# Performance work log

Hardware: AMD Instinct MI355X
Metric: run time of the kernel (lower is better)

## Reference

```python
import jax, jax.numpy as jnp
import numpy as np
import math

B, DIM, H, W = 16, 384, 64, 64
SCALES, HEADS, HID = 4, 4, 32
WIDTH = DIM // SCALES
NUMS = SCALES - 1
PH = PW = 2
LS = 1e-6


def setup_inputs():
    ks = jax.random.split(jax.random.key(0), 20)
    n = lambda i, shape, s=0.02: jax.random.normal(ks[i], shape, jnp.float32) * s
    return {
        'x': jax.random.normal(ks[0], (B, DIM, H, W), jnp.float32),
        'convs_w': n(1, (NUMS, WIDTH, 3, 3)), 'convs_b': n(2, (NUMS, WIDTH)),
        'pos_w': n(3, (DIM, 2 * HID)), 'pos_b': n(4, (DIM,)),
        'ln_xca_w': jnp.ones((DIM,), jnp.float32), 'ln_xca_b': jnp.zeros((DIM,), jnp.float32),
        'gamma_xca': jnp.full((DIM,), LS, jnp.float32),
        'xca_temp': jnp.ones((HEADS, 1, 1), jnp.float32),
        'xca_kv_w': n(5, (2 * DIM, DIM)), 'xca_kv_b': n(6, (2 * DIM,)),
        'xca_proj_w': n(7, (DIM, DIM)), 'xca_proj_b': n(8, (DIM,)),
        'conv_out_w': n(9, (DIM,)), 'conv_out_b': n(10, (DIM,)),
        'wa_kv_w': n(11, (2 * DIM, DIM)), 'wa_kv_b': n(12, (2 * DIM,)),
        'wa_proj_w': n(13, (DIM, DIM)), 'wa_proj_b': n(14, (DIM,)),
        'ln_w': jnp.ones((DIM,), jnp.float32), 'ln_b': jnp.zeros((DIM,), jnp.float32),
        'pw1_w': n(15, (4 * DIM, DIM)), 'pw1_b': n(16, (4 * DIM,)),
        'pw2_w': n(17, (DIM, 4 * DIM)), 'pw2_b': n(18, (DIM,)),
        'gamma': jnp.full((DIM,), LS, jnp.float32),
    }


def layer_norm(x, w, b, eps=1e-6):
    m = jnp.mean(x, -1, keepdims=True)
    v = jnp.mean((x - m) ** 2, -1, keepdims=True)
    return (x - m) * jax.lax.rsqrt(v + eps) * w + b


def l2norm(x, eps=1e-12):  # torch F.normalize over last dim
    return x / jnp.maximum(jnp.linalg.norm(x, axis=-1, keepdims=True), eps)


def dwconv3x3(x, w, b):  # depthwise: w [Cw,3,3]
    out = jax.lax.conv_general_dilated(x, w[:, None], (1, 1), ((1, 1), (1, 1)),
        dimension_numbers=('NCHW', 'OIHW', 'NCHW'), feature_group_count=w.shape[0])
    return out + b[None, :, None, None]


def pos_fourier(pos_w, pos_b):  # -> [H*W, DIM] (batch-independent since mask is all-false)
    scale = 2 * math.pi
    y = jnp.arange(1, H + 1, dtype=jnp.float32)[:, None] / (H + 1e-6) * scale
    xg = jnp.arange(1, W + 1, dtype=jnp.float32)[None, :] / (W + 1e-6) * scale
    y = jnp.broadcast_to(y, (H, W))
    xg = jnp.broadcast_to(xg, (H, W))
    dim_t = jnp.arange(HID, dtype=jnp.float32)
    dim_t = 10000.0 ** (2 * jnp.floor(dim_t / 2) / HID)
    px = xg[..., None] / dim_t
    py = y[..., None] / dim_t
    px = jnp.stack((jnp.sin(px[..., 0::2]), jnp.cos(px[..., 1::2])), -1).reshape(H, W, HID)
    py = jnp.stack((jnp.sin(py[..., 0::2]), jnp.cos(py[..., 1::2])), -1).reshape(H, W, HID)
    pos = jnp.concatenate((py, px), -1)  # [H,W,2*HID]
    return (pos @ pos_w.T + pos_b).reshape(H * W, DIM)


def xca_fn(x, const, kv_w, kv_b, proj_w, proj_b, temp):
    b, n, c = x.shape
    h, hd = HEADS, c // HEADS
    q1 = const.reshape(b, n, h, hd).transpose(0, 2, 3, 1)          # b,h,hd,n
    kv = (x @ kv_w.T + kv_b).reshape(b, n, 2, h, hd).transpose(2, 0, 3, 1, 4)
    k = l2norm(kv[0].transpose(0, 1, 3, 2))                        # b,h,hd,n (L2 over n)
    v = kv[1].transpose(0, 1, 3, 2)                                # b,h,hd,n
    attn = jax.nn.softmax(jnp.einsum('bhcn,bhdn->bhcd', q1, k) * temp, -1)
    out = jnp.einsum('bhcd,bhdn->bhcn', attn, v)
    out = out.transpose(0, 3, 1, 2).reshape(b, n, c)
    return out @ proj_w.T + proj_b


def window_attn(x, const, kv_w, kv_b, proj_w, proj_b):
    b, n, c = x.shape
    h, hd = HEADS, c // HEADS
    kv = (x @ kv_w.T + kv_b).reshape(b, n, 2, h, hd).transpose(2, 0, 3, 1, 4)
    k = l2norm(kv[0].transpose(0, 1, 3, 2))                        # b,h,hd,n
    v = kv[1].transpose(0, 1, 3, 2)                                # b,h,hd,n
    q1 = const.reshape(b, n, 1, h, hd).transpose(2, 0, 3, 1, 4)    # 1,b,h,n,hd (leading 1 kept, as in torch)
    q1 = q1.transpose(0, 1, 2, 4, 3)                               # 1,b,h,hd,n
    logits = jnp.einsum('obhcn,bhdn->obhcd', q1, k)
    attn = 0.5 * logits / math.sqrt(hd) + 0.5 * jax.nn.softmax(logits, -1)
    attn = jax.nn.softmax(attn, -1)
    out = jnp.einsum('obhcd,bhdn->obhcn', attn, v)                 # 1,b,h,hd,n
    out = out.transpose(0, 2, 1, 3, 4).reshape(b, n, c)            # torch .transpose(1,2).reshape(B,N,C)
    return out @ proj_w.T + proj_b


def unfold(x):  # H,W divisible by patch -> no interpolate branch
    b, c = x.shape[0], x.shape[1]
    nph, npw = H // PH, W // PW
    x = x.reshape(b * c * nph, PH, npw, PW).transpose(0, 2, 1, 3)
    x = x.reshape(b, c, nph * npw, PH * PW).transpose(0, 3, 2, 1)
    return x.reshape(b * PH * PW, nph * npw, c)


def fold(x):
    c = x.shape[-1]
    nph, npw = H // PH, W // PW
    x = x.reshape(B, PH * PW, nph * npw, c).transpose(0, 3, 2, 1)
    x = x.reshape(B * c * nph, npw, PH, PW).transpose(0, 2, 1, 3)
    return x.reshape(B, c, nph * PH, npw * PW)


def reference(x, convs_w, convs_b, pos_w, pos_b, ln_xca_w, ln_xca_b, gamma_xca,
              xca_temp, xca_kv_w, xca_kv_b, xca_proj_w, xca_proj_b,
              conv_out_w, conv_out_b, wa_kv_w, wa_kv_b, wa_proj_w, wa_proj_b,
              ln_w, ln_b, pw1_w, pw1_b, pw2_w, pw2_b, gamma):
    inp = x
    # multi-scale depthwise convs (Res2Net style)
    spx = jnp.split(x, SCALES, axis=1)
    outs = []
    sp = spx[0]
    for i in range(NUMS):
        if i > 0:
            sp = sp + spx[i]
        sp = dwconv3x3(sp, convs_w[i], convs_b[i])
        outs.append(sp)
    x = jnp.concatenate(outs + [spx[NUMS]], axis=1)
    N = H * W
    x3 = x.reshape(B, DIM, N).transpose(0, 2, 1)                   # B,N,C
    x3 = x3 + pos_fourier(pos_w, pos_b)[None]
    const = inp.reshape(B, DIM, N).transpose(0, 2, 1)
    x4 = x3 + gamma_xca * xca_fn(layer_norm(x3, ln_xca_w, ln_xca_b), const,
                                 xca_kv_w, xca_kv_b, xca_proj_w, xca_proj_b, xca_temp)
    x4 = x4.reshape(B, H, W, DIM).transpose(0, 3, 1, 2)
    # conv_out: Conv2d(dim,dim,1,groups=dim) == per-channel scale+bias
    x = x4 * conv_out_w[None, :, None, None] + conv_out_b[None, :, None, None]
    x2 = window_attn(unfold(x), unfold(inp), wa_kv_w, wa_kv_b, wa_proj_w, wa_proj_b)
    x = fold(x2).transpose(0, 2, 3, 1)                             # B,H,W,C
    x = layer_norm(x, ln_w, ln_b)
    x = jax.nn.gelu(x @ pw1_w.T + pw1_b, approximate=False)
    x = x @ pw2_w.T + pw2_b
    x = gamma * x
    return inp + x.transpose(0, 3, 1, 2)
```

## Files before the change

kernel.cpp:

```cpp
#include <hip/hip_runtime.h>
#include <math.h>

#define NBATCH 16
#define CDIM   384
#define NPIX   4096
#define HDCH   96
#define NROWS  65536
#define KVHALF 25165824

typedef unsigned short bf16;
typedef __attribute__((ext_vector_type(8))) short short8;
typedef __attribute__((ext_vector_type(4))) float floatx4;

union S8U { short8 v; bf16 u[8]; };

__device__ __forceinline__ float b2f(bf16 u) {
    union { unsigned int i; float f; } c; c.i = ((unsigned int)u) << 16; return c.f;
}
__device__ __forceinline__ bf16 f2b(float f) {
    union { float f; unsigned int i; } c; c.f = f;
    unsigned int r = (c.i + 0x7FFFu + ((c.i >> 16) & 1u)) >> 16;
    return (bf16)r;
}

__device__ __forceinline__ void gload16(const bf16* g, bf16* l) {
    __builtin_amdgcn_global_load_lds(
        (const __attribute__((address_space(1))) unsigned int*)g,
        (__attribute__((address_space(3))) unsigned int*)l, 16, 0, 0);
}

__global__ __launch_bounds__(256) void zero_kernel(float* __restrict__ p) {
    p[blockIdx.x * 256 + threadIdx.x] = 0.0f;
}

__global__ __launch_bounds__(256) void wcvt_kernel(const float* __restrict__ w,
                                                   bf16* __restrict__ o, int n4) {
    int i = blockIdx.x * 256 + threadIdx.x;
    if (i < n4) {
        float4 v = ((const float4*)w)[i];
        ushort4 u;
        u.x = f2b(v.x); u.y = f2b(v.y); u.z = f2b(v.z); u.w = f2b(v.w);
        ((ushort4*)o)[i] = u;
    }
}

__global__ __launch_bounds__(128) void pos_kernel(const float* __restrict__ pos_w,
                                                  const float* __restrict__ pos_b,
                                                  bf16* __restrict__ pos) {
    __shared__ float feat[64];
    int n = blockIdx.x;
    int yi = n >> 6, xi = n & 63;
    int tid = threadIdx.x;
    if (tid < 64) {
        int j = tid & 31;
        int isx = tid >= 32;
        float base = (float)((isx ? xi : yi) + 1);
        float val = base / (64.0f + 1e-6f) * 6.283185307179586f;
        float e = (float)(2 * (j >> 1)) / 32.0f;
        float dt = powf(10000.0f, e);
        float a = val / dt;
        feat[isx * 32 + j] = (j & 1) ? cosf(a) : sinf(a);
    }
    __syncthreads();
    for (int c = tid; c < CDIM; c += 128) {
        float s = pos_b[c];
        const float* wr = pos_w + c * 64;
        #pragma unroll 16
        for (int j = 0; j < 64; ++j) s += feat[j] * wr[j];
        pos[n * CDIM + c] = f2b(s);
    }
}

__global__ __launch_bounds__(256) void dwconv_kernel(const float* __restrict__ xin, int in_ch0,
                                                     const bf16* __restrict__ prev, int prev_ch0,
                                                     const float* __restrict__ w,
                                                     const float* __restrict__ bias,
                                                     bf16* __restrict__ out, int out_ch0) {
    __shared__ float tile[66][66];
    int b = blockIdx.x / 96, c = blockIdx.x % 96;
    const float* ip = xin + (b * CDIM + in_ch0 + c) * NPIX;
    const bf16* pp = prev ? prev + (b * CDIM + prev_ch0 + c) * NPIX : nullptr;
    int tid = threadIdx.x;
    for (int i = tid; i < 66 * 66; i += 256) {
        int yy = i / 66 - 1, xx = i % 66 - 1;
        float v = 0.0f;
        if (yy >= 0 && yy < 64 && xx >= 0 && xx < 64) {
            v = ip[yy * 64 + xx];
            if (pp) v += b2f(pp[yy * 64 + xx]);
        }
        tile[i / 66][i % 66] = v;
    }
    __syncthreads();
    float wc[9];
    #pragma unroll
    for (int j = 0; j < 9; ++j) wc[j] = w[c * 9 + j];
    float b0 = bias[c];
    bf16* op = out + (b * CDIM + out_ch0 + c) * NPIX;
    for (int p = tid; p < NPIX; p += 256) {
        int y = p >> 6, x = p & 63;
        float a = b0;
        #pragma unroll
        for (int dy = 0; dy < 3; ++dy)
            #pragma unroll
            for (int dx = 0; dx < 3; ++dx)
                a += tile[y + dy][x + dx] * wc[dy * 3 + dx];
        op[p] = f2b(a);
    }
}

__global__ __launch_bounds__(256) void convert_last_kernel(const float* __restrict__ x,
                                                           bf16* __restrict__ xcat) {
    int idx = blockIdx.x * 256 + threadIdx.x;
    int b = idx / (96 * 1024);
    int rem = idx % (96 * 1024);
    const float4* src = (const float4*)(x + (b * CDIM + 288) * NPIX);
    float4 v = src[rem];
    ushort4 o;
    o.x = f2b(v.x); o.y = f2b(v.y); o.z = f2b(v.z); o.w = f2b(v.w);
    ((ushort4*)(xcat + (b * CDIM + 288) * NPIX))[rem] = o;
}

__global__ void x3_kernel(const bf16* __restrict__ xcat, const bf16* __restrict__ pos,
                          bf16* __restrict__ x3) {
    __shared__ float t[32][33];
    int c0 = blockIdx.x * 32, n0 = blockIdx.y * 32, b = blockIdx.z;
    int tx = threadIdx.x, ty = threadIdx.y;
    #pragma unroll
    for (int k = 0; k < 4; ++k) {
        int cl = ty + k * 8;
        t[cl][tx] = b2f(xcat[(b * CDIM + c0 + cl) * NPIX + n0 + tx]);
    }
    __syncthreads();
    #pragma unroll
    for (int k = 0; k < 4; ++k) {
        int nl = ty + k * 8;
        x3[(b * NPIX + n0 + nl) * CDIM + c0 + tx] =
            f2b(t[tx][nl] + b2f(pos[(n0 + nl) * CDIM + c0 + tx]));
    }
}

__global__ __launch_bounds__(128) void ln_kernel(const bf16* __restrict__ in,
                                                 const float* __restrict__ w,
                                                 const float* __restrict__ b,
                                                 bf16* __restrict__ out, int map) {
    int r = blockIdx.x;
    int src = r;
    if (map == 1) {
        int bb = r >> 12;
        int p = r & 4095;
        int y = p >> 6, x = p & 63;
        int patch = ((y & 1) << 1) | (x & 1);
        int blk = ((y >> 1) << 5) | (x >> 1);
        src = ((bb << 2) + patch) * 1024 + blk;
    }
    const bf16* row = in + src * CDIM;
    int tid = threadIdx.x;
    float v[3];
    float s1 = 0.0f, s2 = 0.0f;
    #pragma unroll
    for (int i = 0; i < 3; ++i) {
        v[i] = b2f(row[tid + i * 128]);
        s1 += v[i];
        s2 += v[i] * v[i];
    }
    __shared__ float r1[128], r2[128];
    r1[tid] = s1; r2[tid] = s2;
    __syncthreads();
    for (int off = 64; off > 0; off >>= 1) {
        if (tid < off) { r1[tid] += r1[tid + off]; r2[tid] += r2[tid + off]; }
        __syncthreads();
    }
    float mean = r1[0] * (1.0f / 384.0f);
    float var = fmaxf(r2[0] * (1.0f / 384.0f) - mean * mean, 0.0f);
    float rstd = rsqrtf(var + 1e-6f);
    #pragma unroll
    for (int i = 0; i < 3; ++i) {
        int c = tid + i * 128;
        out[r * CDIM + c] = f2b((v[i] - mean) * rstd * w[c] + b[c]);
    }
}

__global__ __launch_bounds__(256) void mfma_gemm_kernel(const bf16* __restrict__ A,
                                                        const bf16* __restrict__ W,
                                                        const float* __restrict__ bias,
                                                        bf16* __restrict__ C,
                                                        int M, int Nout, int K, int mode,
                                                        const bf16* __restrict__ res,
                                                        const float* __restrict__ scalevec,
                                                        int nlog2) {
    __shared__ bf16 As[128][32];
    __shared__ bf16 Bs[128][32];
    int m0 = blockIdx.x * 128;
    int n0 = blockIdx.y * 128;
    int tid = threadIdx.x;
    int wave = tid >> 6, lane = tid & 63;
    int wm = (wave & 1) * 64;
    int wn = (wave >> 1) * 64;
    int quad = lane >> 4;
    int lrow = lane & 15;

    int p0b = wave * 1024 + lane * 16;
    int o0 = p0b ^ (((p0b >> 7) & 3) << 4);
    int r0 = o0 >> 6;
    int ch0 = (o0 >> 4) & 3;

    const bf16* aSrc0 = A + (size_t)(m0 + r0) * K + ch0 * 8;
    const bf16* aSrc1 = A + (size_t)(m0 + r0 + 64) * K + ch0 * 8;
    const bf16* bSrc0 = W + (size_t)(n0 + r0) * K + ch0 * 8;
    const bf16* bSrc1 = W + (size_t)(n0 + r0 + 64) * K + ch0 * 8;
    bf16* lA0 = &As[0][0] + wave * 512;
    bf16* lA1 = &As[0][0] + 2048 + wave * 512;
    bf16* lB0 = &Bs[0][0] + wave * 512;
    bf16* lB1 = &Bs[0][0] + 2048 + wave * 512;

    int rcol = (quad ^ ((lrow >> 1) & 3)) * 8;

    floatx4 acc[4][4] = {};

    for (int k0 = 0; k0 < K; k0 += 32) {
        __syncthreads();
        gload16(aSrc0 + k0, lA0);
        gload16(aSrc1 + k0, lA1);
        gload16(bSrc0 + k0, lB0);
        gload16(bSrc1 + k0, lB1);
        __syncthreads();
        short8 af[4], bfr[4];
        #pragma unroll
        for (int i = 0; i < 4; ++i)
            af[i] = *(const short8*)(&As[wm + i * 16 + lrow][rcol]);
        #pragma unroll
        for (int j = 0; j < 4; ++j)
            bfr[j] = *(const short8*)(&Bs[wn + j * 16 + lrow][rcol]);
        #pragma unroll
        for (int i = 0; i < 4; ++i)
            #pragma unroll
            for (int j = 0; j < 4; ++j)
                acc[i][j] = __builtin_amdgcn_mfma_f32_16x16x32_bf16(af[i], bfr[j], acc[i][j], 0, 0, 0);
    }

    if (mode == 3) {
        int nmask = (1 << nlog2) - 1;
        #pragma unroll
        for (int i = 0; i < 4; ++i) {
            int rowb = m0 + wm + i * 16 + quad * 4;
            int bb = rowb >> nlog2, tok = rowb & nmask;
            #pragma unroll
            for (int j = 0; j < 4; ++j) {
                int col = n0 + wn + j * 16 + lrow;
                float bv = bias[col];
                if (col < 384) {
                    ushort4 o;
                    o.x = f2b(acc[i][j][0] + bv);
                    o.y = f2b(acc[i][j][1] + bv);
                    o.z = f2b(acc[i][j][2] + bv);
                    o.w = f2b(acc[i][j][3] + bv);
                    *(ushort4*)(C + ((((size_t)bb * 384 + col) << nlog2) | (size_t)tok)) = o;
                } else {
                    bf16* vp = C + KVHALF + (size_t)rowb * 384 + (col - 384);
                    #pragma unroll
                    for (int r = 0; r < 4; ++r)
                        vp[(size_t)r * 384] = f2b(acc[i][j][r] + bv);
                }
            }
        }
        return;
    }

    #pragma unroll
    for (int i = 0; i < 4; ++i) {
        int rowb = m0 + wm + i * 16 + quad * 4;
        #pragma unroll
        for (int j = 0; j < 4; ++j) {
            int col = n0 + wn + j * 16 + lrow;
            float bv = bias[col];
            #pragma unroll
            for (int r = 0; r < 4; ++r) {
                int row = rowb + r;
                float v = acc[i][j][r] + bv;
                if (mode == 1) {
                    v = 0.5f * v * (1.0f + erff(v * 0.70710678118654752f));
                } else if (mode == 2) {
                    v = b2f(res[(size_t)row * Nout + col]) + scalevec[col] * v;
                }
                C[(size_t)row * Nout + col] = f2b(v);
            }
        }
    }
}

__global__ __launch_bounds__(256) void knormsq2_kernel(const bf16* __restrict__ KT,
                                                       float* __restrict__ outk, int n_len) {
    int row = blockIdx.x;
    const bf16* p = KT + (size_t)row * n_len;
    int tid = threadIdx.x;
    float s = 0.0f;
    for (int i = tid * 8; i < n_len; i += 256 * 8) {
        S8U t; t.v = *(const short8*)(p + i);
        #pragma unroll
        for (int j = 0; j < 8; ++j) { float f = b2f(t.u[j]); s += f * f; }
    }
    __shared__ float red[256];
    red[tid] = s;
    __syncthreads();
    for (int off = 128; off > 0; off >>= 1) {
        if (tid < off) red[tid] += red[tid + off];
        __syncthreads();
    }
    if (tid == 0) outk[row] = red[0];
}

__global__ __launch_bounds__(256) void chan_qk_mfma(const float* __restrict__ qf,
                                                    const bf16* __restrict__ qb,
                                                    const bf16* __restrict__ KT,
                                                    float* __restrict__ Sg,
                                                    int n_len, int nchunks, int mode) {
    int pair = blockIdx.x / nchunks, ck = blockIdx.x % nchunks;
    int bi = pair >> 2, h = pair & 3;
    int koff = h * HDCH;
    int chunk = n_len / nchunks;
    int nbeg = ck * chunk;
    int tid = threadIdx.x;
    int wave = tid >> 6, lane = tid & 63;
    int lr = lane & 15, q = lane >> 4;
    int c0 = (wave & 1) * 48;
    int d0 = (wave >> 1) * 48;
    floatx4 acc[3][3] = {};
    const size_t qbase = (size_t)(bi * CDIM + koff) * n_len;
    const bf16* kbase = KT + (size_t)(bi * CDIM + koff) * n_len;
    for (int nn = 0; nn < chunk; nn += 32) {
        int n0 = nbeg + nn + q * 8;
        short8 af[3], bfr[3];
        if (mode == 0) {
            #pragma unroll
            for (int i = 0; i < 3; ++i) {
                const float* qp = qf + qbase + (size_t)(c0 + i * 16 + lr) * n_len + n0;
                float4 f0 = *(const float4*)qp;
                float4 f1 = *(const float4*)(qp + 4);
                S8U t;
                t.u[0] = f2b(f0.x); t.u[1] = f2b(f0.y); t.u[2] = f2b(f0.z); t.u[3] = f2b(f0.w);
                t.u[4] = f2b(f1.x); t.u[5] = f2b(f1.y); t.u[6] = f2b(f1.z); t.u[7] = f2b(f1.w);
                af[i] = t.v;
            }
        } else {
            #pragma unroll
            for (int i = 0; i < 3; ++i)
                af[i] = *(const short8*)(qb + qbase + (size_t)(c0 + i * 16 + lr) * n_len + n0);
        }
        #pragma unroll
        for (int j = 0; j < 3; ++j)
            bfr[j] = *(const short8*)(kbase + (size_t)(d0 + j * 16 + lr) * n_len + n0);
        #pragma unroll
        for (int i = 0; i < 3; ++i)
            #pragma unroll
            for (int j = 0; j < 3; ++j)
                acc[i][j] = __builtin_amdgcn_mfma_f32_16x16x32_bf16(af[i], bfr[j], acc[i][j], 0, 0, 0);
    }
    float* Sp = Sg + (size_t)pair * 9216;
    #pragma unroll
    for (int i = 0; i < 3; ++i) {
        int rowb = c0 + i * 16 + q * 4;
        #pragma unroll
        for (int j = 0; j < 3; ++j) {
            int col = d0 + j * 16 + lr;
            #pragma unroll
            for (int r = 0; r < 4; ++r)
                atomicAdd(&Sp[(rowb + r) * 96 + col], acc[i][j][r]);
        }
    }
}

__global__ __launch_bounds__(128) void chan_softmax_kernel(const float* __restrict__ Sg,
                                                           const float* __restrict__ knsq,
                                                           const float* __restrict__ temp,
                                                           bf16* __restrict__ Sb,
                                                           int mode) {
    __shared__ float knrm[96];
    int pair = blockIdx.x;
    int bi = pair >> 2, h = pair & 3;
    int tid = threadIdx.x;
    if (tid < 96)
        knrm[tid] = 1.0f / fmaxf(sqrtf(knsq[bi * CDIM + h * HDCH + tid]), 1e-12f);
    __syncthreads();
    if (tid >= 96) return;
    const float* Sr = Sg + (size_t)pair * 9216 + tid * 96;
    bf16* Ob = Sb + (size_t)pair * 9216 + tid * 96;
    if (mode == 0) {
        float tv = temp[h];
        float m = -1e30f;
        for (int d = 0; d < 96; ++d) m = fmaxf(m, Sr[d] * knrm[d] * tv);
        float s = 0.0f;
        for (int d = 0; d < 96; ++d) s += expf(Sr[d] * knrm[d] * tv - m);
        float inv = 1.0f / s;
        for (int d = 0; d < 96; ++d) Ob[d] = f2b(expf(Sr[d] * knrm[d] * tv - m) * inv);
    } else {
        const float RSQ = 0.10206207261596575f;
        float m1 = -1e30f;
        for (int d = 0; d < 96; ++d) m1 = fmaxf(m1, Sr[d] * knrm[d]);
        float s1 = 0.0f;
        for (int d = 0; d < 96; ++d) s1 += expf(Sr[d] * knrm[d] - m1);
        float inv1 = 1.0f / s1;
        float m2 = -1e30f;
        for (int d = 0; d < 96; ++d) {
            float l = Sr[d] * knrm[d];
            float a = 0.5f * l * RSQ + 0.5f * expf(l - m1) * inv1;
            m2 = fmaxf(m2, a);
        }
        float s2 = 0.0f;
        for (int d = 0; d < 96; ++d) {
            float l = Sr[d] * knrm[d];
            float a = 0.5f * l * RSQ + 0.5f * expf(l - m1) * inv1;
            s2 += expf(a - m2);
        }
        float inv2 = 1.0f / s2;
        for (int d = 0; d < 96; ++d) {
            float l = Sr[d] * knrm[d];
            float a = 0.5f * l * RSQ + 0.5f * expf(l - m1) * inv1;
            Ob[d] = f2b(expf(a - m2) * inv2);
        }
    }
}

#define PVTN 256
__global__ __launch_bounds__(256) void chan_pv_mfma(const bf16* __restrict__ Sb,
                                                    const bf16* __restrict__ V,
                                                    bf16* __restrict__ out,
                                                    int n_len, int mode) {
    int nch = n_len / PVTN;
    int pair = blockIdx.x / nch, ck = blockIdx.x % nch;
    int bi = pair >> 2, h = pair & 3;
    int koff = h * HDCH;
    int tid = threadIdx.x;
    int wave = tid >> 6, lane = tid & 63;
    int lr = lane & 15, q = lane >> 4;
    const bf16* Ab = Sb + (size_t)pair * 9216;
    short8 af[6][3];
    #pragma unroll
    for (int i = 0; i < 6; ++i)
        #pragma unroll
        for (int kt = 0; kt < 3; ++kt)
            af[i][kt] = *(const short8*)(Ab + (i * 16 + lr) * 96 + kt * 32 + q * 8);
    const bf16* vb = V + (size_t)bi * n_len * 384 + koff;
    int nbase = ck * PVTN + wave * 16;
    #pragma unroll
    for (int s = 0; s < 4; ++s) {
        int n = nbase + s * 64 + lr;
        short8 bfr[3];
        #pragma unroll
        for (int kt = 0; kt < 3; ++kt)
            bfr[kt] = *(const short8*)(vb + (size_t)n * 384 + kt * 32 + q * 8);
        floatx4 acc[6] = {};
        #pragma unroll
        for (int kt = 0; kt < 3; ++kt)
            #pragma unroll
            for (int i = 0; i < 6; ++i)
                acc[i] = __builtin_amdgcn_mfma_f32_16x16x32_bf16(af[i][kt], bfr[kt], acc[i], 0, 0, 0);
        if (mode == 0) {
            bf16* op = out + (size_t)(bi * n_len + n) * CDIM + koff;
            #pragma unroll
            for (int i = 0; i < 6; ++i) {
                ushort4 o;
                o.x = f2b(acc[i][0]); o.y = f2b(acc[i][1]);
                o.z = f2b(acc[i][2]); o.w = f2b(acc[i][3]);
                *(ushort4*)(op + i * 16 + q * 4) = o;
            }
        } else {
            #pragma unroll
            for (int i = 0; i < 6; ++i) {
                int cb = i * 16 + q * 4;
                #pragma unroll
                for (int r = 0; r < 4; ++r)
                    out[(size_t)((h * 64 + bi) * HDCH + cb + r) * n_len + n] = f2b(acc[i][r]);
            }
        }
    }
}

__global__ __launch_bounds__(256) void unfold_cu_kernel(const float* __restrict__ xin,
                                                        bf16* __restrict__ cu) {
    int idx = blockIdx.x * 256 + threadIdx.x;
    int b2 = idx / (CDIM * 1024);
    int rem = idx % (CDIM * 1024);
    int ch = rem >> 10, blk = rem & 1023;
    int b = b2 >> 2, patch = b2 & 3;
    int y = ((blk >> 5) << 1) | (patch >> 1);
    int x = ((blk & 31) << 1) | (patch & 1);
    cu[idx] = f2b(xin[(size_t)(b * CDIM + ch) * NPIX + (y << 6) + x]);
}

__global__ __launch_bounds__(256) void unfold_xu_kernel(const bf16* __restrict__ x4,
                                                        const float* __restrict__ cw,
                                                        const float* __restrict__ cb,
                                                        bf16* __restrict__ xu) {
    int idx = blockIdx.x * 256 + threadIdx.x;
    int row = idx / CDIM, ch = idx % CDIM;
    int b2 = row >> 10, blk = row & 1023;
    int b = b2 >> 2, patch = b2 & 3;
    int y = ((blk >> 5) << 1) | (patch >> 1);
    int x = ((blk & 31) << 1) | (patch & 1);
    xu[idx] = f2b(b2f(x4[(size_t)(b * NPIX + (y << 6) + x) * CDIM + ch]) * cw[ch] + cb[ch]);
}

__global__ void out_kernel(const float* __restrict__ xin, const bf16* __restrict__ fin,
                           const float* __restrict__ gamma, float* __restrict__ outp) {
    __shared__ float t[32][33];
    int c0 = blockIdx.x * 32, p0 = blockIdx.y * 32, b = blockIdx.z;
    int tx = threadIdx.x, ty = threadIdx.y;
    #pragma unroll
    for (int k = 0; k < 4; ++k) {
        int pl = ty + k * 8;
        t[pl][tx] = b2f(fin[(size_t)(b * NPIX + p0 + pl) * CDIM + c0 + tx]);
    }
    __syncthreads();
    #pragma unroll
    for (int k = 0; k < 4; ++k) {
        int cl = ty + k * 8;
        size_t addr = (size_t)(b * CDIM + c0 + cl) * NPIX + p0 + tx;
        outp[addr] = xin[addr] + gamma[c0 + cl] * t[tx][cl];
    }
}

extern "C" void kernel_launch(void* const* d_in, const int* in_sizes, int n_in,
                              void* d_out, int out_size, void* d_ws, size_t ws_size,
                              hipStream_t stream) {
    (void)in_sizes; (void)n_in; (void)out_size; (void)ws_size;
    const float* x         = (const float*)d_in[0];
    const float* convs_w   = (const float*)d_in[1];
    const float* convs_b   = (const float*)d_in[2];
    const float* pos_w     = (const float*)d_in[3];
    const float* pos_b     = (const float*)d_in[4];
    const float* ln_xca_w  = (const float*)d_in[5];
    const float* ln_xca_b  = (const float*)d_in[6];
    const float* gamma_xca = (const float*)d_in[7];
    const float* xca_temp  = (const float*)d_in[8];
    const float* xca_kv_w  = (const float*)d_in[9];
    const float* xca_kv_b  = (const float*)d_in[10];
    const float* xca_proj_w= (const float*)d_in[11];
    const float* xca_proj_b= (const float*)d_in[12];
    const float* conv_out_w= (const float*)d_in[13];
    const float* conv_out_b= (const float*)d_in[14];
    const float* wa_kv_w   = (const float*)d_in[15];
    const float* wa_kv_b   = (const float*)d_in[16];
    const float* wa_proj_w = (const float*)d_in[17];
    const float* wa_proj_b = (const float*)d_in[18];
    const float* ln_w      = (const float*)d_in[19];
    const float* ln_b      = (const float*)d_in[20];
    const float* pw1_w     = (const float*)d_in[21];
    const float* pw1_b     = (const float*)d_in[22];
    const float* pw2_w     = (const float*)d_in[23];
    const float* pw2_b     = (const float*)d_in[24];
    const float* gamma     = (const float*)d_in[25];
    float* out = (float*)d_out;

    bf16* pos = (bf16*)d_ws;
    bf16* P1  = pos + 1572864;
    bf16* P2  = P1 + 25165824;
    bf16* P3  = P2 + 25165824;
    float* knsq    = (float*)(P3 + 50331648);
    float* knsq_wa = knsq + 6144;
    float* S_xca   = knsq_wa + 24576;
    float* S_wa    = S_xca + 589824;

    bf16* wbufA = pos + 589824;
    bf16* wbufB = pos;

    zero_kernel<<<11640, 256, 0, stream>>>(knsq);

    pos_kernel<<<4096, 128, 0, stream>>>(pos_w, pos_b, pos);

    dwconv_kernel<<<NBATCH * 96, 256, 0, stream>>>(x,   0, nullptr, 0,  convs_w,        convs_b,       P1, 0);
    dwconv_kernel<<<NBATCH * 96, 256, 0, stream>>>(x,  96, P1,      0,  convs_w + 864,  convs_b + 96,  P1, 96);
    dwconv_kernel<<<NBATCH * 96, 256, 0, stream>>>(x, 192, P1,     96,  convs_w + 1728, convs_b + 192, P1, 192);
    convert_last_kernel<<<6144, 256, 0, stream>>>(x, P1);

    x3_kernel<<<dim3(12, 128, NBATCH), dim3(32, 8), 0, stream>>>(P1, pos, P2);

    ln_kernel<<<NROWS, 128, 0, stream>>>(P2, ln_xca_w, ln_xca_b, P1, 0);
    wcvt_kernel<<<288, 256, 0, stream>>>(xca_kv_w, wbufA, 73728);
    mfma_gemm_kernel<<<dim3(512, 6), 256, 0, stream>>>(P1, wbufA, xca_kv_b, P3,
                                                       NROWS, 768, 384, 3, nullptr, nullptr, 12);
    knormsq2_kernel<<<6144, 256, 0, stream>>>(P3, knsq, 4096);
    chan_qk_mfma<<<512, 256, 0, stream>>>(x, nullptr, P3, S_xca, 4096, 8, 0);
    chan_softmax_kernel<<<64, 128, 0, stream>>>(S_xca, knsq, xca_temp, pos, 0);
    chan_pv_mfma<<<1024, 256, 0, stream>>>(pos, P3 + KVHALF, P1, 4096, 0);
    wcvt_kernel<<<144, 256, 0, stream>>>(xca_proj_w, wbufA, 36864);
    mfma_gemm_kernel<<<dim3(512, 3), 256, 0, stream>>>(P1, wbufA, xca_proj_b, P3,
                                                       NROWS, 384, 384, 2, P2, gamma_xca, 0);

    unfold_cu_kernel<<<98304, 256, 0, stream>>>(x, P2);
    unfold_xu_kernel<<<98304, 256, 0, stream>>>(P3, conv_out_w, conv_out_b, P1);
    wcvt_kernel<<<288, 256, 0, stream>>>(wa_kv_w, wbufA, 73728);
    mfma_gemm_kernel<<<dim3(512, 6), 256, 0, stream>>>(P1, wbufA, wa_kv_b, P3,
                                                       NROWS, 768, 384, 3, nullptr, nullptr, 10);
    knormsq2_kernel<<<24576, 256, 0, stream>>>(P3, knsq_wa, 1024);
    chan_qk_mfma<<<512, 256, 0, stream>>>(nullptr, P2, P3, S_wa, 1024, 2, 1);
    chan_softmax_kernel<<<256, 128, 0, stream>>>(S_wa, knsq_wa, nullptr, P2, 1);
    chan_pv_mfma<<<1024, 256, 0, stream>>>(P2, P3 + KVHALF, P1, 1024, 1);
    wcvt_kernel<<<144, 256, 0, stream>>>(wa_proj_w, wbufA, 36864);
    mfma_gemm_kernel<<<dim3(512, 3), 256, 0, stream>>>(P1, wbufA, wa_proj_b, P2,
                                                       NROWS, 384, 384, 0, nullptr, nullptr, 0);

    ln_kernel<<<NROWS, 128, 0, stream>>>(P2, ln_w, ln_b, P1, 1);
    wcvt_kernel<<<576, 256, 0, stream>>>(pw1_w, wbufA, 147456);
    wcvt_kernel<<<576, 256, 0, stream>>>(pw2_w, wbufB, 147456);
    for (int ch = 0; ch < 4; ++ch) {
        mfma_gemm_kernel<<<dim3(128, 12), 256, 0, stream>>>(P1 + (size_t)ch * 16384 * 384, wbufA, pw1_b,
                                                            P3, 16384, 1536, 384, 1, nullptr, nullptr, 0);
        mfma_gemm_kernel<<<dim3(128, 3), 256, 0, stream>>>(P3, wbufB, pw2_b,
                                                           P2 + (size_t)ch * 16384 * 384, 16384, 384, 1536,
                                                           0, nullptr, nullptr, 0);
    }

    out_kernel<<<dim3(12, 128, NBATCH), dim3(32, 8), 0, stream>>>(x, P2, gamma, out);
}
```

Before: 1.360 ms.

## Triple-buffer GEMM LDS tiles and halve MLP chunk count

The shared MFMA GEMM kernel now keeps three LDS stages, issuing global-to-LDS loads two K-tiles ahead and using vmcnt waits with a single barrier per iteration in place of two syncthreads around each load. This overlaps global memory latency with MFMA work. The MLP pw1/pw2 GEMMs are now run in 2 chunks of 32768 rows instead of 4 of 16384, giving larger grids and fewer launches, at the cost of a larger P3 intermediate buffer (32768x1536 bf16) that must fit in the allocation. LDS use per block triples, which may lower occupancy.

```diff
diff --git a/kernel.cpp b/kernel.cpp
--- a/kernel.cpp
+++ b/kernel.cpp
@@ -188,8 +188,8 @@
                                                         const bf16* __restrict__ res,
                                                         const float* __restrict__ scalevec,
                                                         int nlog2) {
-    __shared__ bf16 As[128][32];
-    __shared__ bf16 Bs[128][32];
+    __shared__ bf16 As[3][128][32];
+    __shared__ bf16 Bs[3][128][32];
     int m0 = blockIdx.x * 128;
     int n0 = blockIdx.y * 128;
     int tid = threadIdx.x;
@@ -208,35 +208,51 @@
     const bf16* aSrc1 = A + (size_t)(m0 + r0 + 64) * K + ch0 * 8;
     const bf16* bSrc0 = W + (size_t)(n0 + r0) * K + ch0 * 8;
     const bf16* bSrc1 = W + (size_t)(n0 + r0 + 64) * K + ch0 * 8;
-    bf16* lA0 = &As[0][0] + wave * 512;
-    bf16* lA1 = &As[0][0] + 2048 + wave * 512;
-    bf16* lB0 = &Bs[0][0] + wave * 512;
-    bf16* lB1 = &Bs[0][0] + 2048 + wave * 512;
+    bf16* lA0 = &As[0][0][0] + wave * 512;
+    bf16* lA1 = &As[0][0][0] + 2048 + wave * 512;
+    bf16* lB0 = &Bs[0][0][0] + wave * 512;
+    bf16* lB1 = &Bs[0][0][0] + 2048 + wave * 512;
 
     int rcol = (quad ^ ((lrow >> 1) & 3)) * 8;
+    int NT = K >> 5;
+
+#define STAGE(bi_, t_) do { int _off = (bi_) * 4096; int _kk = (t_) * 32; \
+        gload16(aSrc0 + _kk, lA0 + _off); \
+        gload16(aSrc1 + _kk, lA1 + _off); \
+        gload16(bSrc0 + _kk, lB0 + _off); \
+        gload16(bSrc1 + _kk, lB1 + _off); } while (0)
 
     floatx4 acc[4][4] = {};
 
-    for (int k0 = 0; k0 < K; k0 += 32) {
-        __syncthreads();
-        gload16(aSrc0 + k0, lA0);
-        gload16(aSrc1 + k0, lA1);
-        gload16(bSrc0 + k0, lB0);
-        gload16(bSrc1 + k0, lB1);
-        __syncthreads();
+    STAGE(0, 0);
+    STAGE(1, 1);
+    asm volatile("s_waitcnt vmcnt(4)" ::: "memory");
+    __builtin_amdgcn_s_barrier();
+    __builtin_amdgcn_sched_barrier(0);
+
+    for (int t = 0; t < NT; ++t) {
+        int bi = t % 3;
+        if (t + 2 < NT) STAGE((t + 2) % 3, t + 2);
         short8 af[4], bfr[4];
         #pragma unroll
         for (int i = 0; i < 4; ++i)
-            af[i] = *(const short8*)(&As[wm + i * 16 + lrow][rcol]);
+            af[i] = *(const short8*)(&As[bi][wm + i * 16 + lrow][rcol]);
         #pragma unroll
         for (int j = 0; j < 4; ++j)
-            bfr[j] = *(const short8*)(&Bs[wn + j * 16 + lrow][rcol]);
+            bfr[j] = *(const short8*)(&Bs[bi][wn + j * 16 + lrow][rcol]);
         #pragma unroll
         for (int i = 0; i < 4; ++i)
             #pragma unroll
             for (int j = 0; j < 4; ++j)
                 acc[i][j] = __builtin_amdgcn_mfma_f32_16x16x32_bf16(af[i], bfr[j], acc[i][j], 0, 0, 0);
-    }
+        if (t + 1 < NT) {
+            if (t + 2 < NT) asm volatile("s_waitcnt vmcnt(4)" ::: "memory");
+            else            asm volatile("s_waitcnt vmcnt(0)" ::: "memory");
+            __builtin_amdgcn_s_barrier();
+            __builtin_amdgcn_sched_barrier(0);
+        }
+    }
+#undef STAGE
 
     if (mode == 3) {
         int nmask = (1 << nlog2) - 1;
@@ -602,11 +618,11 @@
     ln_kernel<<<NROWS, 128, 0, stream>>>(P2, ln_w, ln_b, P1, 1);
     wcvt_kernel<<<576, 256, 0, stream>>>(pw1_w, wbufA, 147456);
     wcvt_kernel<<<576, 256, 0, stream>>>(pw2_w, wbufB, 147456);
-    for (int ch = 0; ch < 4; ++ch) {
-        mfma_gemm_kernel<<<dim3(128, 12), 256, 0, stream>>>(P1 + (size_t)ch * 16384 * 384, wbufA, pw1_b,
-                                                            P3, 16384, 1536, 384, 1, nullptr, nullptr, 0);
-        mfma_gemm_kernel<<<dim3(128, 3), 256, 0, stream>>>(P3, wbufB, pw2_b,
-                                                           P2 + (size_t)ch * 16384 * 384, 16384, 384, 1536,
+    for (int ch = 0; ch < 2; ++ch) {
+        mfma_gemm_kernel<<<dim3(256, 12), 256, 0, stream>>>(P1 + (size_t)ch * 32768 * 384, wbufA, pw1_b,
+                                                            P3, 32768, 1536, 384, 1, nullptr, nullptr, 0);
+        mfma_gemm_kernel<<<dim3(256, 3), 256, 0, stream>>>(P3, wbufB, pw2_b,
+                                                           P2 + (size_t)ch * 32768 * 384, 32768, 384, 1536,
                                                            0, nullptr, nullptr, 0);
     }
 
```

Measured after the change: 1.301 ms. 4.4% less time.
